# Performance work log

Measured on AMD Instinct MI355X. Metric: run time of the kernel, lower is better.

## Reference

```python
import jax, jax.numpy as jnp
import numpy as np

DIM_IN, DIM_OUT, DIM_INNER = 1024, 1024, 512

def setup_inputs() -> dict:
    key = jax.random.key(0)
    k1, k2, k3, k4 = jax.random.split(key, 4)
    x = jax.random.normal(k1, (4, 2048, DIM_IN), dtype=jnp.float32)
    # nn.Linear weights stored as [out, in]; init ~ U(-1/sqrt(in), 1/sqrt(in))
    w_qkv = jax.random.uniform(k2, (DIM_INNER * 3, DIM_IN), dtype=jnp.float32,
                               minval=-1.0, maxval=1.0) / np.sqrt(DIM_IN)
    w_out = jax.random.uniform(k3, (DIM_OUT, DIM_INNER), dtype=jnp.float32,
                               minval=-1.0, maxval=1.0) / np.sqrt(DIM_INNER)
    b_out = jax.random.uniform(k4, (DIM_OUT,), dtype=jnp.float32,
                               minval=-1.0, maxval=1.0) / np.sqrt(DIM_INNER)
    return {"x": x, "w_qkv": w_qkv, "w_out": w_out, "b_out": b_out}

def reference(x, w_qkv, w_out, b_out):
    scale = DIM_INNER ** -0.5
    qkv = jnp.einsum('bnd,ed->bne', x, w_qkv)  # [b, n, 3*dim_inner]
    q, k, v = jnp.split(qkv, 3, axis=-1)
    sim = jnp.einsum('bid,bjd->bij', q, k) * scale
    n = sim.shape[-1]
    causal = jnp.tril(jnp.ones((n, n), dtype=bool))  # True = keep
    sim = jnp.where(causal[None], sim, -jnp.finfo(sim.dtype).max)
    attn = jax.nn.softmax(sim, axis=-1)
    out = jnp.einsum('bij,bjd->bid', attn, v)
    return jnp.einsum('bnd,od->bno', out, w_out) + b_out
```

## Files before the change

### kernel.cpp

```cpp
#include <hip/hip_runtime.h>
#include <math.h>


typedef __attribute__((ext_vector_type(8))) short bf16x8_t;
typedef __attribute__((ext_vector_type(4))) float f32x4_t;

__device__ __forceinline__ unsigned short f2bf(float f) {
  unsigned int u = __float_as_uint(f);
  u = (u + 0x7FFFu + ((u >> 16) & 1u)) >> 16;
  return (unsigned short)u;
}
__device__ __forceinline__ float bf2f(unsigned short h) {
  return __uint_as_float(((unsigned int)h) << 16);
}

template <int N>
__device__ __forceinline__ void wait_vmcnt() {
  if constexpr (N == 0) asm volatile("s_waitcnt vmcnt(0)" ::: "memory");
  else if constexpr (N == 3) asm volatile("s_waitcnt vmcnt(3)" ::: "memory");
  else if constexpr (N == 4) asm volatile("s_waitcnt vmcnt(4)" ::: "memory");
  else if constexpr (N == 5) asm volatile("s_waitcnt vmcnt(5)" ::: "memory");
  else if constexpr (N == 6) asm volatile("s_waitcnt vmcnt(6)" ::: "memory");
}

__global__ __launch_bounds__(256) void cvt_all(
    const float* __restrict__ x, unsigned short* __restrict__ xb, int nx,
    const float* __restrict__ w1, unsigned short* __restrict__ w1b, int n1,
    const float* __restrict__ w2, unsigned short* __restrict__ w2b, int n2) {
  const int stride = gridDim.x * blockDim.x * 4;
  const int t0 = (blockIdx.x * blockDim.x + threadIdx.x) * 4;
  for (int i = t0; i < nx; i += stride) {
    float4 f = *(const float4*)(x + i);
    ushort4 u;
    u.x = f2bf(f.x); u.y = f2bf(f.y); u.z = f2bf(f.z); u.w = f2bf(f.w);
    *(ushort4*)(xb + i) = u;
  }
  for (int i = t0; i < n1; i += stride) {
    float4 f = *(const float4*)(w1 + i);
    ushort4 u;
    u.x = f2bf(f.x); u.y = f2bf(f.y); u.z = f2bf(f.z); u.w = f2bf(f.w);
    *(ushort4*)(w1b + i) = u;
  }
  for (int i = t0; i < n2; i += stride) {
    float4 f = *(const float4*)(w2 + i);
    ushort4 u;
    u.x = f2bf(f.x); u.y = f2bf(f.y); u.z = f2bf(f.z); u.w = f2bf(f.w);
    *(ushort4*)(w2b + i) = u;
  }
}

__global__ __launch_bounds__(256) void softmax_causal(unsigned short* __restrict__ sim) {
  const int lane = threadIdx.x & 63;
  const int rowg = blockIdx.x * 4 + (threadIdx.x >> 6);
  const int i = rowg & 2047;
  unsigned short* row = sim + (size_t)rowg * 2048;
  const int nv = i + 1;
  const int tb = ((i >> 7) + 1) << 7;
  const int nc = (nv + 255) >> 8;
  const int ns = (tb + 255) >> 8;

  float v[32];
  float m = -1e30f;
#pragma unroll
  for (int c = 0; c < 8; ++c) {
    if (c < nc) {
      const int j0 = c * 256 + lane * 4;
      ushort4 u = *(const ushort4*)(row + j0);
      float f0 = bf2f(u.x), f1 = bf2f(u.y), f2 = bf2f(u.z), f3 = bf2f(u.w);
      v[c * 4 + 0] = (j0 + 0 < nv) ? f0 : -1e30f;
      v[c * 4 + 1] = (j0 + 1 < nv) ? f1 : -1e30f;
      v[c * 4 + 2] = (j0 + 2 < nv) ? f2 : -1e30f;
      v[c * 4 + 3] = (j0 + 3 < nv) ? f3 : -1e30f;
      m = fmaxf(m, fmaxf(fmaxf(v[c * 4], v[c * 4 + 1]), fmaxf(v[c * 4 + 2], v[c * 4 + 3])));
    }
  }
#pragma unroll
  for (int s = 32; s >= 1; s >>= 1) m = fmaxf(m, __shfl_xor(m, s));
  float sum = 0.f;
#pragma unroll
  for (int c = 0; c < 8; ++c) {
    if (c < nc) {
#pragma unroll
      for (int e = 0; e < 4; ++e) {
        float p = __expf(v[c * 4 + e] - m);
        v[c * 4 + e] = p;
        sum += p;
      }
    }
  }
#pragma unroll
  for (int s = 32; s >= 1; s >>= 1) sum += __shfl_xor(sum, s);
  const float inv = 1.0f / sum;
#pragma unroll
  for (int c = 0; c < 8; ++c) {
    if (c < ns) {
      const int j0 = c * 256 + lane * 4;
      ushort4 u;
      if (c < nc) {
        u.x = f2bf(v[c * 4 + 0] * inv);
        u.y = f2bf(v[c * 4 + 1] * inv);
        u.z = f2bf(v[c * 4 + 2] * inv);
        u.w = f2bf(v[c * 4 + 3] * inv);
      } else {
        u.x = u.y = u.z = u.w = 0;
      }
      *(ushort4*)(row + j0) = u;
    }
  }
}

template <int EPI, int BM, int BN>
__global__ __launch_bounds__(256) void gemm_bt(
    const unsigned short* __restrict__ A, const unsigned short* __restrict__ B,
    int M, int N, int K, long strideA, long strideB, int klim, int causal,
    void* __restrict__ O0, void* __restrict__ O1, void* __restrict__ O2,
    const float* __restrict__ bias, float qscale) {
  const int bm = blockIdx.x, bn = blockIdx.y, bz = blockIdx.z;
  if (causal && bn > bm) return;
  const int tid = threadIdx.x, lane = tid & 63, wave = tid >> 6;
  const int wr = wave >> 1, wc = wave & 1;
  constexpr int FM = BM / 32, FN = BN / 32;
  constexpr int AR = BM / 64, BR = BN / 64;
  constexpr int L = AR + BR;

  __shared__ alignas(16) unsigned short As[3][BM * 32];
  __shared__ alignas(16) unsigned short Bs[3][BN * 32];

  const unsigned short* Ab = A + (size_t)bz * strideA + (size_t)bm * BM * K;
  const unsigned short* Bb = B + (size_t)bz * strideB + (size_t)bn * BN * K;

  const int kmax = klim ? min(K, (bm + 1) * BM) : K;
  const int nkt = kmax >> 5;

  auto stage = [&](int buf, int kt) {
    const int loff = tid * 16;
#pragma unroll
    for (int i = 0; i < AR; ++i) {
      const int o = i * 4096 + loff;
      const int r = o >> 6;
      const int sl = ((o >> 4) & 3) ^ ((r >> 1) & 3);
      __builtin_amdgcn_global_load_lds(
          (const __attribute__((address_space(1))) void*)(
              (const char*)(Ab + (size_t)r * K) + (size_t)kt * 64 + sl * 16),
          (__attribute__((address_space(3))) void*)((char*)As[buf] + o), 16, 0, 0);
    }
#pragma unroll
    for (int i = 0; i < BR; ++i) {
      const int o = i * 4096 + loff;
      const int r = o >> 6;
      const int sl = ((o >> 4) & 3) ^ ((r >> 1) & 3);
      __builtin_amdgcn_global_load_lds(
          (const __attribute__((address_space(1))) void*)(
              (const char*)(Bb + (size_t)r * K) + (size_t)kt * 64 + sl * 16),
          (__attribute__((address_space(3))) void*)((char*)Bs[buf] + o), 16, 0, 0);
    }
  };

  f32x4_t acc[FM][FN] = {};

  stage(0, 0);
  if (nkt > 1) stage(1, 1);
  int cur = 0;
  for (int kt = 0; kt < nkt; ++kt) {
    if (kt + 1 < nkt) wait_vmcnt<L>();
    else wait_vmcnt<0>();
    __builtin_amdgcn_s_barrier();

    bf16x8_t av[FM], bv[FN];
#pragma unroll
    for (int f = 0; f < FM; ++f) {
      const int row = wr * (BM / 2) + f * 16 + (lane & 15);
      const int sp = (lane >> 4) ^ ((row >> 1) & 3);
      av[f] = *(const bf16x8_t*)((const char*)As[cur] + row * 64 + sp * 16);
    }
#pragma unroll
    for (int f = 0; f < FN; ++f) {
      const int row = wc * (BN / 2) + f * 16 + (lane & 15);
      const int sp = (lane >> 4) ^ ((row >> 1) & 3);
      bv[f] = *(const bf16x8_t*)((const char*)Bs[cur] + row * 64 + sp * 16);
    }
    if (kt + 2 < nkt) {
      int nb = cur + 2;
      if (nb >= 3) nb -= 3;
      stage(nb, kt + 2);
    }
    __builtin_amdgcn_s_setprio(1);
#pragma unroll
    for (int fi = 0; fi < FM; ++fi)
#pragma unroll
      for (int fj = 0; fj < FN; ++fj)
        acc[fi][fj] = __builtin_amdgcn_mfma_f32_16x16x32_bf16(av[fi], bv[fj], acc[fi][fj], 0, 0, 0);
    __builtin_amdgcn_s_setprio(0);
    cur = (cur + 1 == 3) ? 0 : cur + 1;
  }

#pragma unroll
  for (int fi = 0; fi < FM; ++fi) {
    const int row_l = wr * (BM / 2) + fi * 16 + ((lane >> 4) << 2);
#pragma unroll
    for (int fj = 0; fj < FN; ++fj) {
      const int col = bn * BN + wc * (BN / 2) + fj * 16 + (lane & 15);
      if constexpr (EPI == 0) {
        const int row0 = bm * BM + row_l;
        if (col < 512) {
#pragma unroll
          for (int r = 0; r < 4; ++r)
            ((unsigned short*)O0)[(size_t)(row0 + r) * 512 + col] =
                f2bf(acc[fi][fj][r] * qscale);
        } else if (col < 1024) {
#pragma unroll
          for (int r = 0; r < 4; ++r)
            ((unsigned short*)O1)[(size_t)(row0 + r) * 512 + (col - 512)] =
                f2bf(acc[fi][fj][r]);
        } else {
          const int e = col - 1024;
          const int b = row0 >> 11, n0 = row0 & 2047;
          ushort4 u;
          u.x = f2bf(acc[fi][fj][0]);
          u.y = f2bf(acc[fi][fj][1]);
          u.z = f2bf(acc[fi][fj][2]);
          u.w = f2bf(acc[fi][fj][3]);
          *(ushort4*)((unsigned short*)O2 + ((size_t)b * 512 + e) * 2048 + n0) = u;
        }
      } else {
#pragma unroll
        for (int r = 0; r < 4; ++r) {
          const int row = bm * BM + row_l + r;
          float v = acc[fi][fj][r];
          if constexpr (EPI == 1) {
            ((unsigned short*)O0)[(size_t)bz * 2048 * 2048 + (size_t)row * 2048 + col] = f2bf(v);
          } else if constexpr (EPI == 2) {
            ((unsigned short*)O0)[(size_t)bz * 2048 * 512 + (size_t)row * 512 + col] = f2bf(v);
          } else {
            ((float*)O0)[(size_t)row * 1024 + col] = v + bias[col];
          }
        }
      }
    }
  }
}

extern "C" void kernel_launch(void* const* d_in, const int* in_sizes, int n_in,
                              void* d_out, int out_size, void* d_ws, size_t ws_size,
                              hipStream_t stream) {
  const float* x = (const float*)d_in[0];
  const float* w_qkv = (const float*)d_in[1];
  const float* w_out = (const float*)d_in[2];
  const float* b_out = (const float*)d_in[3];
  float* out = (float*)d_out;

  char* ws = (char*)d_ws;
  size_t off = 0;
  auto alloc = [&](size_t bytes) {
    size_t o = off;
    off += (bytes + 255) & ~(size_t)255;
    return o;
  };
  unsigned short* xb = (unsigned short*)(ws + alloc((size_t)8192 * 1024 * 2));
  unsigned short* wqkvb = (unsigned short*)(ws + alloc((size_t)1536 * 1024 * 2));
  unsigned short* woutb = (unsigned short*)(ws + alloc((size_t)1024 * 512 * 2));
  unsigned short* qb = (unsigned short*)(ws + alloc((size_t)8192 * 512 * 2));
  unsigned short* kb = (unsigned short*)(ws + alloc((size_t)8192 * 512 * 2));
  unsigned short* vtb = (unsigned short*)(ws + alloc((size_t)8192 * 512 * 2));
  unsigned short* sim = (unsigned short*)(ws + alloc((size_t)4 * 2048 * 2048 * 2));
  unsigned short* ao = (unsigned short*)(ws + alloc((size_t)8192 * 512 * 2));

  const float scale = 1.0f / sqrtf(512.0f);

  cvt_all<<<2048, 256, 0, stream>>>(x, xb, 8192 * 1024, w_qkv, wqkvb, 1536 * 1024,
                                    w_out, woutb, 1024 * 512);

  gemm_bt<0, 128, 128><<<dim3(64, 12, 1), 256, 0, stream>>>(
      xb, wqkvb, 8192, 1536, 1024, 0, 0, 0, 0, qb, kb, vtb, nullptr, scale);

  gemm_bt<1, 128, 128><<<dim3(16, 16, 4), 256, 0, stream>>>(
      qb, kb, 2048, 2048, 512, (long)2048 * 512, (long)2048 * 512,
      0, 1, sim, nullptr, nullptr, nullptr, 0.f);

  softmax_causal<<<2048, 256, 0, stream>>>(sim);

  gemm_bt<2, 128, 64><<<dim3(16, 8, 4), 256, 0, stream>>>(
      sim, vtb, 2048, 512, 2048, (long)2048 * 2048, (long)512 * 2048,
      1, 0, ao, nullptr, nullptr, nullptr, 0.f);

  gemm_bt<3, 128, 128><<<dim3(64, 8, 1), 256, 0, stream>>>(
      ao, woutb, 8192, 1024, 512, 0, 0, 0, 0, out, nullptr, nullptr, b_out, 0.f);
}
```

Measured before the change: 134.2 us.

## Fuse fp32-to-bf16 conversion of x into QKV GEMM and reverse PV block order

```diff
diff --git a/kernel.cpp b/kernel.cpp
--- a/kernel.cpp
+++ b/kernel.cpp
@@ -17,24 +17,15 @@
 template <int N>
 __device__ __forceinline__ void wait_vmcnt() {
   if constexpr (N == 0) asm volatile("s_waitcnt vmcnt(0)" ::: "memory");
-  else if constexpr (N == 3) asm volatile("s_waitcnt vmcnt(3)" ::: "memory");
   else if constexpr (N == 4) asm volatile("s_waitcnt vmcnt(4)" ::: "memory");
-  else if constexpr (N == 5) asm volatile("s_waitcnt vmcnt(5)" ::: "memory");
   else if constexpr (N == 6) asm volatile("s_waitcnt vmcnt(6)" ::: "memory");
 }
 
-__global__ __launch_bounds__(256) void cvt_all(
-    const float* __restrict__ x, unsigned short* __restrict__ xb, int nx,
+__global__ __launch_bounds__(256) void cvt_w(
     const float* __restrict__ w1, unsigned short* __restrict__ w1b, int n1,
     const float* __restrict__ w2, unsigned short* __restrict__ w2b, int n2) {
   const int stride = gridDim.x * blockDim.x * 4;
   const int t0 = (blockIdx.x * blockDim.x + threadIdx.x) * 4;
-  for (int i = t0; i < nx; i += stride) {
-    float4 f = *(const float4*)(x + i);
-    ushort4 u;
-    u.x = f2bf(f.x); u.y = f2bf(f.y); u.z = f2bf(f.z); u.w = f2bf(f.w);
-    *(ushort4*)(xb + i) = u;
-  }
   for (int i = t0; i < n1; i += stride) {
     float4 f = *(const float4*)(w1 + i);
     ushort4 u;
@@ -109,13 +100,145 @@
   }
 }
 
-template <int EPI, int BM, int BN>
+__global__ __launch_bounds__(256) void qkv_gemm(
+    const float* __restrict__ X, const unsigned short* __restrict__ B,
+    unsigned short* __restrict__ Q, unsigned short* __restrict__ Kc,
+    unsigned short* __restrict__ VT, float qscale) {
+  constexpr int BM = 128, BN = 128, K = 1024;
+  constexpr int FM = 4, FN = 4;
+  constexpr int nkt = K / 32;
+  const int bm = blockIdx.x, bn = blockIdx.y;
+  const int tid = threadIdx.x, lane = tid & 63, wave = tid >> 6;
+  const int wr = wave >> 1, wc = wave & 1;
+
+  __shared__ alignas(16) unsigned short As[3][BM * 32];
+  __shared__ alignas(16) unsigned short Bs[3][BN * 32];
+
+  const float* Xb = X + (size_t)bm * BM * K;
+  const unsigned short* Bb = B + (size_t)bn * BN * K;
+
+  const int ar = tid >> 1, ah = tid & 1;
+  const float* asrc = Xb + (size_t)ar * K + ah * 16;
+  const int asw = (ar >> 1) & 3;
+  char* arow = (char*)nullptr;
+
+  float4 arA[4], arB[4];
+
+  auto aloadA = [&](int kt) {
+#pragma unroll
+    for (int j = 0; j < 4; ++j) arA[j] = *(const float4*)(asrc + kt * 32 + j * 4);
+  };
+  auto aloadB = [&](int kt) {
+#pragma unroll
+    for (int j = 0; j < 4; ++j) arB[j] = *(const float4*)(asrc + kt * 32 + j * 4);
+  };
+  auto awrite = [&](int buf, const float4* a) {
+    bf16x8_t lo, hi;
+#pragma unroll
+    for (int j = 0; j < 2; ++j) {
+      lo[j * 4 + 0] = (short)f2bf(a[j].x);
+      lo[j * 4 + 1] = (short)f2bf(a[j].y);
+      lo[j * 4 + 2] = (short)f2bf(a[j].z);
+      lo[j * 4 + 3] = (short)f2bf(a[j].w);
+      hi[j * 4 + 0] = (short)f2bf(a[j + 2].x);
+      hi[j * 4 + 1] = (short)f2bf(a[j + 2].y);
+      hi[j * 4 + 2] = (short)f2bf(a[j + 2].z);
+      hi[j * 4 + 3] = (short)f2bf(a[j + 2].w);
+    }
+    char* base = (char*)As[buf] + ar * 64;
+    *(bf16x8_t*)(base + ((2 * ah + 0) ^ asw) * 16) = lo;
+    *(bf16x8_t*)(base + ((2 * ah + 1) ^ asw) * 16) = hi;
+  };
+  auto bstage = [&](int buf, int kt) {
+    const int loff = tid * 16;
+#pragma unroll
+    for (int i = 0; i < 2; ++i) {
+      const int o = i * 4096 + loff;
+      const int r = o >> 6;
+      const int sl = ((o >> 4) & 3) ^ ((r >> 1) & 3);
+      __builtin_amdgcn_global_load_lds(
+          (const __attribute__((address_space(1))) void*)(
+              (const char*)(Bb + (size_t)r * K) + (size_t)kt * 64 + sl * 16),
+          (__attribute__((address_space(3))) void*)((char*)Bs[buf] + o), 16, 0, 0);
+    }
+  };
+
+  f32x4_t acc[FM][FN] = {};
+
+  aloadA(0); bstage(0, 0);
+  aloadB(1); bstage(1, 1);
+  int cur = 0;
+  for (int kt = 0; kt < nkt; ++kt) {
+    if (kt + 1 < nkt) wait_vmcnt<6>();
+    else wait_vmcnt<0>();
+    if ((kt & 1) == 0) awrite(cur, arA); else awrite(cur, arB);
+    asm volatile("s_waitcnt lgkmcnt(0)" ::: "memory");
+    __builtin_amdgcn_s_barrier();
+    if (kt + 2 < nkt) {
+      if ((kt & 1) == 0) aloadA(kt + 2); else aloadB(kt + 2);
+      int nb = cur + 2;
+      if (nb >= 3) nb -= 3;
+      bstage(nb, kt + 2);
+    }
+    bf16x8_t av[FM], bv[FN];
+#pragma unroll
+    for (int f = 0; f < FM; ++f) {
+      const int row = wr * 64 + f * 16 + (lane & 15);
+      const int sp = (lane >> 4) ^ ((row >> 1) & 3);
+      av[f] = *(const bf16x8_t*)((const char*)As[cur] + row * 64 + sp * 16);
+    }
+#pragma unroll
+    for (int f = 0; f < FN; ++f) {
+      const int row = wc * 64 + f * 16 + (lane & 15);
+      const int sp = (lane >> 4) ^ ((row >> 1) & 3);
+      bv[f] = *(const bf16x8_t*)((const char*)Bs[cur] + row * 64 + sp * 16);
+    }
+    __builtin_amdgcn_s_setprio(1);
+#pragma unroll
+    for (int fi = 0; fi < FM; ++fi)
+#pragma unroll
+      for (int fj = 0; fj < FN; ++fj)
+        acc[fi][fj] = __builtin_amdgcn_mfma_f32_16x16x32_bf16(av[fi], bv[fj], acc[fi][fj], 0, 0, 0);
+    __builtin_amdgcn_s_setprio(0);
+    cur = (cur + 1 == 3) ? 0 : cur + 1;
+  }
+
+#pragma unroll
+  for (int fi = 0; fi < FM; ++fi) {
+    const int row_l = wr * 64 + fi * 16 + ((lane >> 4) << 2);
+#pragma unroll
+    for (int fj = 0; fj < FN; ++fj) {
+      const int col = bn * BN + wc * 64 + fj * 16 + (lane & 15);
+      const int row0 = bm * BM + row_l;
+      if (col < 512) {
+#pragma unroll
+        for (int r = 0; r < 4; ++r)
+          Q[(size_t)(row0 + r) * 512 + col] = f2bf(acc[fi][fj][r] * qscale);
+      } else if (col < 1024) {
+#pragma unroll
+        for (int r = 0; r < 4; ++r)
+          Kc[(size_t)(row0 + r) * 512 + (col - 512)] = f2bf(acc[fi][fj][r]);
+      } else {
+        const int e = col - 1024;
+        const int b = row0 >> 11, n0 = row0 & 2047;
+        ushort4 u;
+        u.x = f2bf(acc[fi][fj][0]);
+        u.y = f2bf(acc[fi][fj][1]);
+        u.z = f2bf(acc[fi][fj][2]);
+        u.w = f2bf(acc[fi][fj][3]);
+        *(ushort4*)(VT + ((size_t)b * 512 + e) * 2048 + n0) = u;
+      }
+    }
+  }
+}
+
+template <int EPI, int BM, int BN, int REV>
 __global__ __launch_bounds__(256) void gemm_bt(
     const unsigned short* __restrict__ A, const unsigned short* __restrict__ B,
     int M, int N, int K, long strideA, long strideB, int klim, int causal,
-    void* __restrict__ O0, void* __restrict__ O1, void* __restrict__ O2,
-    const float* __restrict__ bias, float qscale) {
-  const int bm = blockIdx.x, bn = blockIdx.y, bz = blockIdx.z;
+    void* __restrict__ O0, const float* __restrict__ bias) {
+  const int bm = REV ? (gridDim.x - 1 - blockIdx.x) : blockIdx.x;
+  const int bn = blockIdx.y, bz = blockIdx.z;
   if (causal && bn > bm) return;
   const int tid = threadIdx.x, lane = tid & 63, wave = tid >> 6;
   const int wr = wave >> 1, wc = wave & 1;
@@ -200,40 +323,16 @@
 #pragma unroll
     for (int fj = 0; fj < FN; ++fj) {
       const int col = bn * BN + wc * (BN / 2) + fj * 16 + (lane & 15);
-      if constexpr (EPI == 0) {
-        const int row0 = bm * BM + row_l;
-        if (col < 512) {
-#pragma unroll
-          for (int r = 0; r < 4; ++r)
-            ((unsigned short*)O0)[(size_t)(row0 + r) * 512 + col] =
-                f2bf(acc[fi][fj][r] * qscale);
-        } else if (col < 1024) {
-#pragma unroll
-          for (int r = 0; r < 4; ++r)
-            ((unsigned short*)O1)[(size_t)(row0 + r) * 512 + (col - 512)] =
-                f2bf(acc[fi][fj][r]);
+#pragma unroll
+      for (int r = 0; r < 4; ++r) {
+        const int row = bm * BM + row_l + r;
+        float v = acc[fi][fj][r];
+        if constexpr (EPI == 1) {
+          ((unsigned short*)O0)[(size_t)bz * 2048 * 2048 + (size_t)row * 2048 + col] = f2bf(v);
+        } else if constexpr (EPI == 2) {
+          ((unsigned short*)O0)[(size_t)bz * 2048 * 512 + (size_t)row * 512 + col] = f2bf(v);
         } else {
-          const int e = col - 1024;
-          const int b = row0 >> 11, n0 = row0 & 2047;
-          ushort4 u;
-          u.x = f2bf(acc[fi][fj][0]);
-          u.y = f2bf(acc[fi][fj][1]);
-          u.z = f2bf(acc[fi][fj][2]);
-          u.w = f2bf(acc[fi][fj][3]);
-          *(ushort4*)((unsigned short*)O2 + ((size_t)b * 512 + e) * 2048 + n0) = u;
-        }
-      } else {
-#pragma unroll
-        for (int r = 0; r < 4; ++r) {
-          const int row = bm * BM + row_l + r;
-          float v = acc[fi][fj][r];
-          if constexpr (EPI == 1) {
-            ((unsigned short*)O0)[(size_t)bz * 2048 * 2048 + (size_t)row * 2048 + col] = f2bf(v);
-          } else if constexpr (EPI == 2) {
-            ((unsigned short*)O0)[(size_t)bz * 2048 * 512 + (size_t)row * 512 + col] = f2bf(v);
-          } else {
-            ((float*)O0)[(size_t)row * 1024 + col] = v + bias[col];
-          }
+          ((float*)O0)[(size_t)row * 1024 + col] = v + bias[col];
         }
       }
     }
@@ -256,7 +355,6 @@
     off += (bytes + 255) & ~(size_t)255;
     return o;
   };
-  unsigned short* xb = (unsigned short*)(ws + alloc((size_t)8192 * 1024 * 2));
   unsigned short* wqkvb = (unsigned short*)(ws + alloc((size_t)1536 * 1024 * 2));
   unsigned short* woutb = (unsigned short*)(ws + alloc((size_t)1024 * 512 * 2));
   unsigned short* qb = (unsigned short*)(ws + alloc((size_t)8192 * 512 * 2));
@@ -267,22 +365,20 @@
 
   const float scale = 1.0f / sqrtf(512.0f);
 
-  cvt_all<<<2048, 256, 0, stream>>>(x, xb, 8192 * 1024, w_qkv, wqkvb, 1536 * 1024,
-                                    w_out, woutb, 1024 * 512);
-
-  gemm_bt<0, 128, 128><<<dim3(64, 12, 1), 256, 0, stream>>>(
-      xb, wqkvb, 8192, 1536, 1024, 0, 0, 0, 0, qb, kb, vtb, nullptr, scale);
-
-  gemm_bt<1, 128, 128><<<dim3(16, 16, 4), 256, 0, stream>>>(
+  cvt_w<<<512, 256, 0, stream>>>(w_qkv, wqkvb, 1536 * 1024, w_out, woutb, 1024 * 512);
+
+  qkv_gemm<<<dim3(64, 12), 256, 0, stream>>>(x, wqkvb, qb, kb, vtb, scale);
+
+  gemm_bt<1, 128, 128, 0><<<dim3(16, 16, 4), 256, 0, stream>>>(
       qb, kb, 2048, 2048, 512, (long)2048 * 512, (long)2048 * 512,
-      0, 1, sim, nullptr, nullptr, nullptr, 0.f);
+      0, 1, sim, nullptr);
 
   softmax_causal<<<2048, 256, 0, stream>>>(sim);
 
-  gemm_bt<2, 128, 64><<<dim3(16, 8, 4), 256, 0, stream>>>(
+  gemm_bt<2, 128, 64, 1><<<dim3(16, 8, 4), 256, 0, stream>>>(
       sim, vtb, 2048, 512, 2048, (long)2048 * 2048, (long)512 * 2048,
-      1, 0, ao, nullptr, nullptr, nullptr, 0.f);
-
-  gemm_bt<3, 128, 128><<<dim3(64, 8, 1), 256, 0, stream>>>(
-      ao, woutb, 8192, 1024, 512, 0, 0, 0, 0, out, nullptr, nullptr, b_out, 0.f);
-}
+      1, 0, ao, nullptr);
+
+  gemm_bt<3, 128, 128, 0><<<dim3(64, 8, 1), 256, 0, stream>>>(
+      ao, woutb, 8192, 1024, 512, 0, 0, 0, 0, out, b_out);
+}
```

Measured after the change: 188.0 us. 1.4x slower.

## Launch only lower-triangle QK^T tiles and reverse-order PV with 64-row tiles

Applied to the files above, without the earlier changes.

```diff
diff --git a/kernel.cpp b/kernel.cpp
--- a/kernel.cpp
+++ b/kernel.cpp
@@ -19,7 +19,6 @@
   if constexpr (N == 0) asm volatile("s_waitcnt vmcnt(0)" ::: "memory");
   else if constexpr (N == 3) asm volatile("s_waitcnt vmcnt(3)" ::: "memory");
   else if constexpr (N == 4) asm volatile("s_waitcnt vmcnt(4)" ::: "memory");
-  else if constexpr (N == 5) asm volatile("s_waitcnt vmcnt(5)" ::: "memory");
   else if constexpr (N == 6) asm volatile("s_waitcnt vmcnt(6)" ::: "memory");
 }
 
@@ -55,7 +54,7 @@
   const int i = rowg & 2047;
   unsigned short* row = sim + (size_t)rowg * 2048;
   const int nv = i + 1;
-  const int tb = ((i >> 7) + 1) << 7;
+  const int tb = ((i >> 6) + 1) << 6;
   const int nc = (nv + 255) >> 8;
   const int ns = (tb + 255) >> 8;
 
@@ -109,14 +108,25 @@
   }
 }
 
-template <int EPI, int BM, int BN>
+template <int EPI, int BM, int BN, int REV, int TRI>
 __global__ __launch_bounds__(256) void gemm_bt(
     const unsigned short* __restrict__ A, const unsigned short* __restrict__ B,
-    int M, int N, int K, long strideA, long strideB, int klim, int causal,
+    int M, int N, int K, long strideA, long strideB, int klim,
     void* __restrict__ O0, void* __restrict__ O1, void* __restrict__ O2,
     const float* __restrict__ bias, float qscale) {
-  const int bm = blockIdx.x, bn = blockIdx.y, bz = blockIdx.z;
-  if (causal && bn > bm) return;
+  int bm, bn, bz;
+  if constexpr (TRI) {
+    const int bid = blockIdx.x;
+    bm = (int)((sqrtf(8.f * (float)bid + 1.f) - 1.f) * 0.5f);
+    while ((bm + 1) * (bm + 2) / 2 <= bid) ++bm;
+    while (bm * (bm + 1) / 2 > bid) --bm;
+    bn = bid - bm * (bm + 1) / 2;
+    bz = blockIdx.y;
+  } else {
+    bm = REV ? (gridDim.x - 1 - blockIdx.x) : blockIdx.x;
+    bn = blockIdx.y;
+    bz = blockIdx.z;
+  }
   const int tid = threadIdx.x, lane = tid & 63, wave = tid >> 6;
   const int wr = wave >> 1, wc = wave & 1;
   constexpr int FM = BM / 32, FN = BN / 32;
@@ -270,19 +280,19 @@
   cvt_all<<<2048, 256, 0, stream>>>(x, xb, 8192 * 1024, w_qkv, wqkvb, 1536 * 1024,
                                     w_out, woutb, 1024 * 512);
 
-  gemm_bt<0, 128, 128><<<dim3(64, 12, 1), 256, 0, stream>>>(
-      xb, wqkvb, 8192, 1536, 1024, 0, 0, 0, 0, qb, kb, vtb, nullptr, scale);
-
-  gemm_bt<1, 128, 128><<<dim3(16, 16, 4), 256, 0, stream>>>(
+  gemm_bt<0, 128, 128, 0, 0><<<dim3(64, 12, 1), 256, 0, stream>>>(
+      xb, wqkvb, 8192, 1536, 1024, 0, 0, 0, qb, kb, vtb, nullptr, scale);
+
+  gemm_bt<1, 128, 128, 0, 1><<<dim3(136, 4, 1), 256, 0, stream>>>(
       qb, kb, 2048, 2048, 512, (long)2048 * 512, (long)2048 * 512,
-      0, 1, sim, nullptr, nullptr, nullptr, 0.f);
+      0, sim, nullptr, nullptr, nullptr, 0.f);
 
   softmax_causal<<<2048, 256, 0, stream>>>(sim);
 
-  gemm_bt<2, 128, 64><<<dim3(16, 8, 4), 256, 0, stream>>>(
+  gemm_bt<2, 64, 128, 1, 0><<<dim3(32, 4, 4), 256, 0, stream>>>(
       sim, vtb, 2048, 512, 2048, (long)2048 * 2048, (long)512 * 2048,
-      1, 0, ao, nullptr, nullptr, nullptr, 0.f);
-
-  gemm_bt<3, 128, 128><<<dim3(64, 8, 1), 256, 0, stream>>>(
-      ao, woutb, 8192, 1024, 512, 0, 0, 0, 0, out, nullptr, nullptr, b_out, 0.f);
-}
+      1, ao, nullptr, nullptr, nullptr, 0.f);
+
+  gemm_bt<3, 128, 128, 0, 0><<<dim3(64, 8, 1), 256, 0, stream>>>(
+      ao, woutb, 8192, 1024, 512, 0, 0, 0, out, nullptr, nullptr, b_out, 0.f);
+}
```

New measurement: 128.3 us. 1.05x faster.
